# Kernel tuning notes

Measured on AMD Instinct MI355X. Metric: run time of the kernel, lower is better.

The kernel has to match this reference:

```python
import jax, jax.numpy as jnp
import numpy as np

N = 50000        # nodes
E = 800000       # edges (avg degree 16)
G = 512          # graphs in batch
H = 128          # hidden_channels
F = 128          # num_filters
NG = 50          # num_gaussians
NI = 6           # num_interactions
CUTOFF = 10.0


def ssp(x):
    # shifted softplus: softplus(x) - log(2)
    return jax.nn.softplus(x) - jnp.log(2.0).astype(x.dtype)


def setup_inputs() -> dict:
    key = jax.random.key(0)
    ks = jax.random.split(key, 16)
    z = jax.random.randint(ks[0], (N,), 0, 100)
    pos = jax.random.uniform(ks[1], (N, 3), jnp.float32) * 5.0  # box keeps d < cutoff
    batch = jnp.sort(jax.random.randint(ks[2], (N,), 0, G))
    row = jax.random.randint(ks[3], (E,), 0, N)
    off = jax.random.randint(ks[4], (E,), 1, N)
    col = (row + off) % N  # no self loops -> d > 0
    edge_index = jnp.stack([row, col])
    s = 0.1
    emb = jax.random.normal(ks[5], (100, H), jnp.float32) * s
    w1 = jax.random.normal(ks[6], (NI, NG, F), jnp.float32) * s
    b1 = jnp.zeros((NI, F), jnp.float32)
    w2 = jax.random.normal(ks[7], (NI, F, F), jnp.float32) * s
    b2 = jnp.zeros((NI, F), jnp.float32)
    lin1_w = jax.random.normal(ks[8], (NI, H, F), jnp.float32) * s   # no bias
    lin2_w = jax.random.normal(ks[9], (NI, F, H), jnp.float32) * s
    lin2_b = jnp.zeros((NI, H), jnp.float32)
    lin_w = jax.random.normal(ks[10], (NI, H, H), jnp.float32) * s
    lin_b = jnp.zeros((NI, H), jnp.float32)
    out_w1 = jax.random.normal(ks[11], (H, H // 2), jnp.float32) * s
    out_b1 = jnp.zeros((H // 2,), jnp.float32)
    out_w2 = jax.random.normal(ks[12], (H // 2, 1), jnp.float32) * s
    out_b2 = jnp.zeros((1,), jnp.float32)
    return dict(pos=pos, emb=emb, w1=w1, b1=b1, w2=w2, b2=b2,
                lin1_w=lin1_w, lin2_w=lin2_w, lin2_b=lin2_b,
                lin_w=lin_w, lin_b=lin_b,
                out_w1=out_w1, out_b1=out_b1, out_w2=out_w2, out_b2=out_b2,
                z=z, batch=batch, edge_index=edge_index)


def reference(pos, emb, w1, b1, w2, b2, lin1_w, lin2_w, lin2_b, lin_w, lin_b,
              out_w1, out_b1, out_w2, out_b2, z, batch, edge_index):
    row, col = edge_index[0], edge_index[1]  # row = target i, col = source j
    diff = pos[row] - pos[col]               # [E,3]
    d = jnp.sqrt(jnp.sum(diff * diff, axis=-1) + 1e-12)  # [E]

    # Gaussian smearing (PyG): exp(coeff * (d - offset)^2)
    offset = jnp.linspace(0.0, CUTOFF, NG, dtype=jnp.float32)
    coeff = -0.5 / (offset[1] - offset[0]) ** 2
    rbf = jnp.exp(coeff * (d[:, None] - offset) ** 2)  # [E,NG]

    # cosine cutoff
    C = 0.5 * (jnp.cos(d * (jnp.pi / CUTOFF)) + 1.0)    # [E]

    h = emb[z]  # [N,H]
    for i in range(NI):
        # filter network on edge RBF features
        W = ssp(rbf @ w1[i] + b1[i]) @ w2[i] + b2[i]    # [E,F]
        W = W * C[:, None]
        x = h @ lin1_w[i]                               # [N,F]
        msg = x[col] * W                                # gather + modulate [E,F]
        agg = jax.ops.segment_sum(msg, row, num_segments=N)  # scatter-add [N,F]
        x = agg @ lin2_w[i] + lin2_b[i]                 # [N,H]
        x = ssp(x)
        x = x @ lin_w[i] + lin_b[i]
        h = h + x                                       # residual

    h = ssp(h @ out_w1 + out_b1)                        # [N,H//2]
    per_atom = h @ out_w2 + out_b2                      # [N,1]
    energy = jax.ops.segment_sum(per_atom, batch, num_segments=G)  # [G,1]
    return energy
```

## Files before the change

kernel.cpp:

```cpp
#include <hip/hip_runtime.h>
#include <math.h>


constexpr int Nn  = 50000;
constexpr int Ee  = 800000;
constexpr int Gg  = 512;
constexpr int Hh  = 128;
constexpr int NGg = 50;
constexpr int NIi = 6;
constexpr int TS  = 4096;
constexpr float DMAXv = 8.6603f;

typedef short bf16x8 __attribute__((ext_vector_type(8)));
typedef float f32x4  __attribute__((ext_vector_type(4)));

__device__ __forceinline__ float ssp(float v) {
    return log1pf(__expf(-fabsf(v))) + fmaxf(v, 0.0f) - 0.69314718056f;
}
__device__ __forceinline__ unsigned short f2bf(float f) {
    unsigned int u = __float_as_uint(f);
    u += 0x7fffu + ((u >> 16) & 1u);
    return (unsigned short)(u >> 16);
}
__device__ __forceinline__ float bf2f(unsigned int h) {
    return __uint_as_float(h << 16);
}

__global__ void k_embed(const float* __restrict__ emb, const int* __restrict__ z,
                        float* __restrict__ h) {
    int tid = blockIdx.x * 256 + threadIdx.x;
    int n = tid >> 7, f = tid & 127;
    h[tid] = emb[z[n] * Hh + f];
}

__global__ void k_hist(const int* __restrict__ ei, int* __restrict__ counts) {
    int e = blockIdx.x * 256 + threadIdx.x;
    if (e >= Ee) return;
    atomicAdd(&counts[ei[e]], 1);
}

__global__ __launch_bounds__(1024) void k_scan(const int* __restrict__ counts,
                                               int* __restrict__ offsets) {
    __shared__ int s[1024];
    constexpr int CH = (Nn + 1023) / 1024;
    int t = threadIdx.x;
    int beg = t * CH, end = beg + CH; if (end > Nn) end = Nn;
    int sum = 0;
    for (int i = beg; i < end; ++i) sum += counts[i];
    s[t] = sum;
    __syncthreads();
    for (int off = 1; off < 1024; off <<= 1) {
        int v = (t >= off) ? s[t - off] : 0;
        __syncthreads();
        s[t] += v;
        __syncthreads();
    }
    int base = (t == 0) ? 0 : s[t - 1];
    for (int i = beg; i < end; ++i) {
        offsets[i] = base;
        base += counts[i];
    }
    if (t == 1023) offsets[Nn] = base;
}

__global__ void k_scatter(const int* __restrict__ ei, const float* __restrict__ pos,
                          int* __restrict__ cursor, int2* __restrict__ payload,
                          float inv_step) {
    int e = blockIdx.x * 256 + threadIdx.x;
    if (e >= Ee) return;
    int r = ei[e], c = ei[Ee + e];
    float dx = pos[3 * r    ] - pos[3 * c    ];
    float dy = pos[3 * r + 1] - pos[3 * c + 1];
    float dz = pos[3 * r + 2] - pos[3 * c + 2];
    float d = sqrtf(dx * dx + dy * dy + dz * dz + 1e-12f);
    float u = d * inv_step;
    if (u > (float)(TS - 1) - 5e-4f) u = (float)(TS - 1) - 5e-4f;
    int p = atomicAdd(&cursor[r], 1);
    payload[p] = make_int2(c, __float_as_int(u));
}

__global__ void k_pack(const float* __restrict__ lin1, const float* __restrict__ lin2,
                       const float* __restrict__ lin3, const float* __restrict__ ow1,
                       short* __restrict__ Wp) {
    int o = blockIdx.x * 256 + threadIdx.x;
    if (o < 18 * 16384) {
        int m = o >> 14, r = o & 16383;
        int k = (r >> 7) & 127, c = r & 127;
        int i = m / 3, which = m % 3;
        const float* src = which == 0 ? lin1 : (which == 1 ? lin2 : lin3);
        float v = src[(size_t)i * 16384 + k * 128 + c];
        int nt = c >> 4, lc = c & 15, kk = k >> 5, kg = (k >> 3) & 3, e = k & 7;
        int l = kg * 16 + lc;
        Wp[(size_t)m * 16384 + ((nt * 4 + kk) * 64 + l) * 8 + e] = (short)f2bf(v);
    } else {
        int r = o - 18 * 16384;
        int k = r >> 6, c = r & 63;
        float v = ow1[k * 64 + c];
        int nt = c >> 4, lc = c & 15, kk = k >> 5, kg = (k >> 3) & 3, e = k & 7;
        int l = kg * 16 + lc;
        Wp[(size_t)18 * 16384 + ((nt * 4 + kk) * 64 + l) * 8 + e] = (short)f2bf(v);
    }
}

__global__ __launch_bounds__(256) void k_table(
        const float* __restrict__ w1, const float* __restrict__ b1,
        const float* __restrict__ w2, const float* __restrict__ b2,
        unsigned short* __restrict__ T, float step) {
    __shared__ unsigned int w2p[64 * 128];
    __shared__ unsigned int w1p[25 * 128];
    __shared__ float rbf_s[2][NGg];
    __shared__ float tb[2][128];
    int tid = threadIdx.x;
    for (int i = tid; i < 64 * 128; i += 256) {
        int k2 = i >> 7, f = i & 127;
        unsigned int lo = f2bf(w2[(2 * k2) * 128 + f]);
        unsigned int hi = f2bf(w2[(2 * k2 + 1) * 128 + f]);
        w2p[i] = lo | (hi << 16);
    }
    for (int i = tid; i < 25 * 128; i += 256) {
        int k2 = i >> 7, f = i & 127;
        unsigned int lo = f2bf(w1[(2 * k2) * 128 + f]);
        unsigned int hi = f2bf(w1[(2 * k2 + 1) * 128 + f]);
        w1p[i] = lo | (hi << 16);
    }
    int jj = tid >> 7, f = tid & 127;
    float bb1 = b1[f], bb2 = b2[f];
    for (int p = 0; p < 4; ++p) {
        int j = blockIdx.x * 8 + p * 2 + jj;
        float dj = j * step;
        __syncthreads();
        if (f < NGg) {
            float u = dj - f * (10.0f / 49.0f);
            rbf_s[jj][f] = expf(-12.00500f * u * u);
        }
        __syncthreads();
        float u = bb1;
        for (int k2 = 0; k2 < 25; ++k2) {
            unsigned int wv = w1p[k2 * 128 + f];
            u = fmaf(rbf_s[jj][2 * k2    ], bf2f(wv & 0xffffu), u);
            u = fmaf(rbf_s[jj][2 * k2 + 1], bf2f(wv >> 16), u);
        }
        tb[jj][f] = ssp(u);
        __syncthreads();
        float w = bb2;
        for (int k2 = 0; k2 < 64; ++k2) {
            unsigned int wv = w2p[k2 * 128 + f];
            w = fmaf(tb[jj][2 * k2    ], bf2f(wv & 0xffffu), w);
            w = fmaf(tb[jj][2 * k2 + 1], bf2f(wv >> 16), w);
        }
        float C = 0.5f * (cosf(dj * 0.31415926535f) + 1.0f);
        T[j * 128 + f] = f2bf(w * C);
    }
}

__global__ __launch_bounds__(256) void k_mfma1(
        const float* __restrict__ in, const short* __restrict__ Wp,
        unsigned short* __restrict__ out, int nrows) {
    __shared__ short As[64 * 128];
    int tid = threadIdx.x;
    int base = blockIdx.x * 64;
    const float4* in4 = (const float4*)(in + (size_t)base * 128);
    int lim4 = (nrows - base) * 32;
    for (int i = tid; i < 2048; i += 256) {
        float4 v = make_float4(0.f, 0.f, 0.f, 0.f);
        if (i < lim4) v = in4[i];
        ushort4 o; o.x = f2bf(v.x); o.y = f2bf(v.y); o.z = f2bf(v.z); o.w = f2bf(v.w);
        int row = i >> 5, colg = i & 31;
        int byte = (row * 256 + colg * 8) ^ ((row & 7) << 4);
        *(ushort4*)((char*)As + byte) = o;
    }
    __syncthreads();

    int w = tid >> 6, lane = tid & 63;
    int arow = w * 16 + (lane & 15);
    bf16x8 a[4];
    #pragma unroll
    for (int kk = 0; kk < 4; ++kk) {
        int byte = (arow * 256 + kk * 64 + (lane >> 4) * 16) ^ ((arow & 7) << 4);
        a[kk] = *(const bf16x8*)((const char*)As + byte);
    }
    f32x4 acc[8];
    f32x4 zero = {0.f, 0.f, 0.f, 0.f};
    #pragma unroll
    for (int nt = 0; nt < 8; ++nt) acc[nt] = zero;
    const bf16x8* Wp8 = (const bf16x8*)Wp;
    #pragma unroll
    for (int nt = 0; nt < 8; ++nt)
        #pragma unroll
        for (int kk = 0; kk < 4; ++kk)
            acc[nt] = __builtin_amdgcn_mfma_f32_16x16x32_bf16(
                a[kk], Wp8[(nt * 4 + kk) * 64 + lane], acc[nt], 0, 0, 0);
    #pragma unroll
    for (int nt = 0; nt < 8; ++nt) {
        int col = nt * 16 + (lane & 15);
        #pragma unroll
        for (int r = 0; r < 4; ++r) {
            int row = base + w * 16 + (lane >> 4) * 4 + r;
            if (row < nrows) out[(size_t)row * 128 + col] = f2bf(acc[nt][r]);
        }
    }
}

__global__ __launch_bounds__(256) void k_mfma23(
        const float* __restrict__ agg, const short* __restrict__ W2p,
        const float* __restrict__ b2, const short* __restrict__ W3p,
        const float* __restrict__ b3, float* __restrict__ h, int nrows) {
    __shared__ short As[64 * 128];
    int tid = threadIdx.x;
    int base = blockIdx.x * 64;
    const float4* in4 = (const float4*)(agg + (size_t)base * 128);
    int lim4 = (nrows - base) * 32;
    for (int i = tid; i < 2048; i += 256) {
        float4 v = make_float4(0.f, 0.f, 0.f, 0.f);
        if (i < lim4) v = in4[i];
        ushort4 o; o.x = f2bf(v.x); o.y = f2bf(v.y); o.z = f2bf(v.z); o.w = f2bf(v.w);
        int row = i >> 5, colg = i & 31;
        int byte = (row * 256 + colg * 8) ^ ((row & 7) << 4);
        *(ushort4*)((char*)As + byte) = o;
    }
    __syncthreads();

    int w = tid >> 6, lane = tid & 63;
    int arow = w * 16 + (lane & 15);
    f32x4 zero = {0.f, 0.f, 0.f, 0.f};
    bf16x8 a[4];
    #pragma unroll
    for (int kk = 0; kk < 4; ++kk) {
        int byte = (arow * 256 + kk * 64 + (lane >> 4) * 16) ^ ((arow & 7) << 4);
        a[kk] = *(const bf16x8*)((const char*)As + byte);
    }
    f32x4 acc[8];
    #pragma unroll
    for (int nt = 0; nt < 8; ++nt) acc[nt] = zero;
    const bf16x8* W2p8 = (const bf16x8*)W2p;
    #pragma unroll
    for (int nt = 0; nt < 8; ++nt)
        #pragma unroll
        for (int kk = 0; kk < 4; ++kk)
            acc[nt] = __builtin_amdgcn_mfma_f32_16x16x32_bf16(
                a[kk], W2p8[(nt * 4 + kk) * 64 + lane], acc[nt], 0, 0, 0);

    #pragma unroll
    for (int nt = 0; nt < 8; ++nt) {
        int col = nt * 16 + (lane & 15);
        float bv = b2[col];
        #pragma unroll
        for (int r = 0; r < 4; ++r) {
            int row = w * 16 + (lane >> 4) * 4 + r;
            int byte = (row * 256 + col * 2) ^ ((row & 7) << 4);
            *(unsigned short*)((char*)As + byte) = f2bf(ssp(acc[nt][r] + bv));
        }
    }
    __syncthreads();

    bf16x8 a2[4];
    #pragma unroll
    for (int kk = 0; kk < 4; ++kk) {
        int byte = (arow * 256 + kk * 64 + (lane >> 4) * 16) ^ ((arow & 7) << 4);
        a2[kk] = *(const bf16x8*)((const char*)As + byte);
    }
    f32x4 acc2[8];
    #pragma unroll
    for (int nt = 0; nt < 8; ++nt) acc2[nt] = zero;
    const bf16x8* W3p8 = (const bf16x8*)W3p;
    #pragma unroll
    for (int nt = 0; nt < 8; ++nt)
        #pragma unroll
        for (int kk = 0; kk < 4; ++kk)
            acc2[nt] = __builtin_amdgcn_mfma_f32_16x16x32_bf16(
                a2[kk], W3p8[(nt * 4 + kk) * 64 + lane], acc2[nt], 0, 0, 0);

    #pragma unroll
    for (int nt = 0; nt < 8; ++nt) {
        int col = nt * 16 + (lane & 15);
        float bv3 = b3[col];
        #pragma unroll
        for (int r = 0; r < 4; ++r) {
            int row = base + w * 16 + (lane >> 4) * 4 + r;
            if (row < nrows) {
                float* hp = h + (size_t)row * 128 + col;
                *hp += acc2[nt][r] + bv3;
            }
        }
    }
}

__device__ __forceinline__ void lerp_acc(unsigned int ta, unsigned int tb,
                                         unsigned int xv, float fr, float2& acc) {
    float t0a = bf2f(ta & 0xffffu), t0b = bf2f(ta >> 16);
    float t1a = bf2f(tb & 0xffffu), t1b = bf2f(tb >> 16);
    acc.x = fmaf(bf2f(xv & 0xffffu), fmaf(t1a - t0a, fr, t0a), acc.x);
    acc.y = fmaf(bf2f(xv >> 16),     fmaf(t1b - t0b, fr, t0b), acc.y);
}

__global__ __launch_bounds__(256) void k_agg(
        const int* __restrict__ offs, const int2* __restrict__ payload,
        const unsigned int* __restrict__ xw, const unsigned int* __restrict__ Tw,
        float* __restrict__ agg) {
    int wid = threadIdx.x >> 6, lane = threadIdx.x & 63;
    int n = blockIdx.x * 4 + wid;
    int beg = offs[n], end = offs[n + 1];
    float2 acc = make_float2(0.f, 0.f);
    int e = beg, cnt = end - beg;
    int2 p0, p1, p2, p3;
    if (cnt >= 4) { p0 = payload[e]; p1 = payload[e + 1]; p2 = payload[e + 2]; p3 = payload[e + 3]; }
    while (cnt >= 4) {
        unsigned int c0 = p0.x, c1 = p1.x, c2 = p2.x, c3 = p3.x;
        float u0 = __int_as_float(p0.y), u1 = __int_as_float(p1.y);
        float u2 = __int_as_float(p2.y), u3 = __int_as_float(p3.y);
        int j0 = (int)u0, j1 = (int)u1, j2 = (int)u2, j3 = (int)u3;
        float f0 = u0 - j0, f1 = u1 - j1, f2 = u2 - j2, f3 = u3 - j3;
        unsigned int ta0 = Tw[j0 * 64 + lane], tb0 = Tw[j0 * 64 + 64 + lane];
        unsigned int ta1 = Tw[j1 * 64 + lane], tb1 = Tw[j1 * 64 + 64 + lane];
        unsigned int ta2 = Tw[j2 * 64 + lane], tb2 = Tw[j2 * 64 + 64 + lane];
        unsigned int ta3 = Tw[j3 * 64 + lane], tb3 = Tw[j3 * 64 + 64 + lane];
        unsigned int xv0 = xw[(size_t)c0 * 64 + lane];
        unsigned int xv1 = xw[(size_t)c1 * 64 + lane];
        unsigned int xv2 = xw[(size_t)c2 * 64 + lane];
        unsigned int xv3 = xw[(size_t)c3 * 64 + lane];
        e += 4; cnt -= 4;
        if (cnt >= 4) { p0 = payload[e]; p1 = payload[e + 1]; p2 = payload[e + 2]; p3 = payload[e + 3]; }
        lerp_acc(ta0, tb0, xv0, f0, acc);
        lerp_acc(ta1, tb1, xv1, f1, acc);
        lerp_acc(ta2, tb2, xv2, f2, acc);
        lerp_acc(ta3, tb3, xv3, f3, acc);
    }
    for (; cnt > 0; --cnt, ++e) {
        int2 cur = payload[e];
        float u = __int_as_float(cur.y);
        int j = (int)u;
        float fr = u - (float)j;
        unsigned int ta = Tw[j * 64 + lane];
        unsigned int tb = Tw[j * 64 + 64 + lane];
        unsigned int xv = xw[(size_t)cur.x * 64 + lane];
        lerp_acc(ta, tb, xv, fr, acc);
    }
    ((float2*)agg)[(size_t)n * 64 + lane] = acc;
}

__global__ __launch_bounds__(256) void k_out(
        const float* __restrict__ h, const short* __restrict__ OW1p,
        const float* __restrict__ ob1, const float* __restrict__ ow2,
        const float* __restrict__ ob2, const int* __restrict__ batch,
        float* __restrict__ energy, int nrows) {
    __shared__ short As[64 * 128];
    __shared__ float rowsum[64];
    int tid = threadIdx.x;
    int base = blockIdx.x * 64;
    const float4* in4 = (const float4*)(h + (size_t)base * 128);
    int lim4 = (nrows - base) * 32;
    for (int i = tid; i < 2048; i += 256) {
        float4 v = make_float4(0.f, 0.f, 0.f, 0.f);
        if (i < lim4) v = in4[i];
        ushort4 o; o.x = f2bf(v.x); o.y = f2bf(v.y); o.z = f2bf(v.z); o.w = f2bf(v.w);
        int row = i >> 5, colg = i & 31;
        int byte = (row * 256 + colg * 8) ^ ((row & 7) << 4);
        *(ushort4*)((char*)As + byte) = o;
    }
    __syncthreads();

    int w = tid >> 6, lane = tid & 63;
    int arow = w * 16 + (lane & 15);
    bf16x8 a[4];
    #pragma unroll
    for (int kk = 0; kk < 4; ++kk) {
        int byte = (arow * 256 + kk * 64 + (lane >> 4) * 16) ^ ((arow & 7) << 4);
        a[kk] = *(const bf16x8*)((const char*)As + byte);
    }
    f32x4 acc[4];
    f32x4 zero = {0.f, 0.f, 0.f, 0.f};
    #pragma unroll
    for (int nt = 0; nt < 4; ++nt) acc[nt] = zero;
    const bf16x8* W8 = (const bf16x8*)OW1p;
    #pragma unroll
    for (int nt = 0; nt < 4; ++nt)
        #pragma unroll
        for (int kk = 0; kk < 4; ++kk)
            acc[nt] = __builtin_amdgcn_mfma_f32_16x16x32_bf16(
                a[kk], W8[(nt * 4 + kk) * 64 + lane], acc[nt], 0, 0, 0);

    float p[4] = {0.f, 0.f, 0.f, 0.f};
    #pragma unroll
    for (int nt = 0; nt < 4; ++nt) {
        int col = nt * 16 + (lane & 15);
        float b = ob1[col], wv = ow2[col];
        #pragma unroll
        for (int r = 0; r < 4; ++r) p[r] += ssp(acc[nt][r] + b) * wv;
    }
    #pragma unroll
    for (int m = 1; m < 16; m <<= 1) {
        #pragma unroll
        for (int r = 0; r < 4; ++r) p[r] += __shfl_xor(p[r], m);
    }
    if ((lane & 15) == 0) {
        #pragma unroll
        for (int r = 0; r < 4; ++r) rowsum[w * 16 + (lane >> 4) * 4 + r] = p[r];
    }
    __syncthreads();
    if (tid < 64) {
        int row = base + tid;
        int rc = row < nrows ? row : nrows - 1;
        int g = batch[rc];
        float v = (row < nrows) ? rowsum[tid] + ob2[0] : 0.f;
        #pragma unroll
        for (int off = 1; off < 64; off <<= 1) {
            float vo = __shfl_down(v, off);
            int   go = __shfl_down(g, off);
            if (tid + off < 64 && go == g) v += vo;
        }
        int gp = __shfl_up(g, 1);
        if (row < nrows && (tid == 0 || gp != g))
            unsafeAtomicAdd(&energy[g], v);
    }
}

extern "C" void kernel_launch(void* const* d_in, const int* in_sizes, int n_in,
                              void* d_out, int out_size, void* d_ws, size_t ws_size,
                              hipStream_t stream) {
    const float* pos    = (const float*)d_in[0];
    const float* emb    = (const float*)d_in[1];
    const float* w1     = (const float*)d_in[2];
    const float* b1     = (const float*)d_in[3];
    const float* w2     = (const float*)d_in[4];
    const float* b2     = (const float*)d_in[5];
    const float* lin1_w = (const float*)d_in[6];
    const float* lin2_w = (const float*)d_in[7];
    const float* lin2_b = (const float*)d_in[8];
    const float* lin_w  = (const float*)d_in[9];
    const float* lin_b  = (const float*)d_in[10];
    const float* ow1    = (const float*)d_in[11];
    const float* ob1    = (const float*)d_in[12];
    const float* ow2    = (const float*)d_in[13];
    const float* ob2    = (const float*)d_in[14];
    const int*   z      = (const int*)d_in[15];
    const int*   batch  = (const int*)d_in[16];
    const int*   ei     = (const int*)d_in[17];
    float* energy = (float*)d_out;

    char* ws = (char*)d_ws;
    float*          h       = (float*)ws;          ws += (size_t)Nn * 128 * 4;
    float*          agg     = (float*)ws;          ws += (size_t)Nn * 128 * 4;
    unsigned short* xb      = (unsigned short*)ws; ws += (size_t)Nn * 128 * 2;
    unsigned short* T       = (unsigned short*)ws; ws += (size_t)TS * 128 * 2;
    int2*           payload = (int2*)ws;           ws += (size_t)Ee * 8;
    short*          Wp      = (short*)ws;          ws += ((size_t)18 * 16384 + 8192) * 2;
    int*            counts  = (int*)ws;            ws += (size_t)Nn * 4;
    int*            offsets = (int*)ws;            ws += (size_t)(Nn + 1) * 4;
    int*            cursor  = (int*)ws;            ws += (size_t)Nn * 4;

    float step = DMAXv / (TS - 1);
    float inv_step = (TS - 1) / DMAXv;

    hipMemsetAsync(d_out, 0, Gg * 4, stream);
    hipMemsetAsync(counts, 0, (size_t)Nn * 4, stream);
    k_embed<<<Nn * 128 / 256, 256, 0, stream>>>(emb, z, h);

    k_hist<<<(Ee + 255) / 256, 256, 0, stream>>>(ei, counts);
    k_scan<<<1, 1024, 0, stream>>>(counts, offsets);
    hipMemcpyAsync(cursor, offsets, (size_t)Nn * 4, hipMemcpyDeviceToDevice, stream);
    k_scatter<<<(Ee + 255) / 256, 256, 0, stream>>>(ei, pos, cursor, payload, inv_step);

    k_pack<<<(18 * 16384 + 8192) / 256, 256, 0, stream>>>(lin1_w, lin2_w, lin_w, ow1, Wp);

    int gemm_blocks = (Nn + 63) / 64;
    for (int i = 0; i < NIi; ++i) {
        const short* W1p = Wp + (size_t)(i * 3 + 0) * 16384;
        const short* W2p = Wp + (size_t)(i * 3 + 1) * 16384;
        const short* W3p = Wp + (size_t)(i * 3 + 2) * 16384;
        k_table<<<512, 256, 0, stream>>>(w1 + (size_t)i * NGg * 128, b1 + (size_t)i * 128,
                                         w2 + (size_t)i * 128 * 128, b2 + (size_t)i * 128,
                                         T, step);
        k_mfma1<<<gemm_blocks, 256, 0, stream>>>(h, W1p, xb, Nn);
        k_agg<<<Nn / 4, 256, 0, stream>>>(offsets, payload,
                                          (const unsigned int*)xb, (const unsigned int*)T, agg);
        k_mfma23<<<gemm_blocks, 256, 0, stream>>>(agg, W2p, lin2_b + (size_t)i * Hh,
                                                  W3p, lin_b + (size_t)i * Hh, h, Nn);
    }
    k_out<<<gemm_blocks, 256, 0, stream>>>(h, Wp + (size_t)18 * 16384,
                                           ob1, ow2, ob2, batch, energy, Nn);
}
```

Measured before the change: 1.018 ms.

## Fuse next-layer lin1 GEMM and output head into post-aggregation kernel; parallelize scan

Fuses the next interaction's lin1 projection (and, on the last layer, the output MLP and per-graph energy reduction) into the post-aggregation GEMM kernel. The updated h stays in shared memory as bf16 instead of being re-read by a separate kernel. This removes the k_mfma1 and k_out launches and their full passes over h. The single-block serial prefix scan plus device memcpy is replaced by a three-kernel multi-block scan that writes offsets and cursor together, and the filter-table build is reordered so it runs after aggregation. One cost is that the next layer's lin1 input is now rounded from an fp32 value computed inside the kernel, not re-read from h.

```diff
diff --git a/kernel.cpp b/kernel.cpp
--- a/kernel.cpp
+++ b/kernel.cpp
@@ -9,6 +9,7 @@
 constexpr int NGg = 50;
 constexpr int NIi = 6;
 constexpr int TS  = 4096;
+constexpr int NB  = (Nn + 255) / 256;
 constexpr float DMAXv = 8.6603f;
 
 typedef short bf16x8 __attribute__((ext_vector_type(8)));
@@ -39,28 +40,58 @@
     atomicAdd(&counts[ei[e]], 1);
 }
 
-__global__ __launch_bounds__(1024) void k_scan(const int* __restrict__ counts,
-                                               int* __restrict__ offsets) {
-    __shared__ int s[1024];
-    constexpr int CH = (Nn + 1023) / 1024;
+__global__ __launch_bounds__(256) void k_scanA(const int* __restrict__ counts,
+                                               int* __restrict__ incl,
+                                               int* __restrict__ bsum) {
+    int t = blockIdx.x * 256 + threadIdx.x;
+    int lane = threadIdx.x & 63, wv = threadIdx.x >> 6;
+    int c = (t < Nn) ? counts[t] : 0;
+    int v = c;
+    #pragma unroll
+    for (int off = 1; off < 64; off <<= 1) {
+        int u = __shfl_up(v, off);
+        if (lane >= off) v += u;
+    }
+    __shared__ int ws[4];
+    if (lane == 63) ws[wv] = v;
+    __syncthreads();
+    if (threadIdx.x == 0) {
+        int s = 0;
+        #pragma unroll
+        for (int i = 0; i < 4; ++i) { int x = ws[i]; ws[i] = s; s += x; }
+        bsum[blockIdx.x] = s;
+    }
+    __syncthreads();
+    v += ws[wv];
+    if (t < Nn) incl[t] = v;
+}
+
+__global__ __launch_bounds__(256) void k_scanB(int* __restrict__ bsum) {
+    __shared__ int s[256];
     int t = threadIdx.x;
-    int beg = t * CH, end = beg + CH; if (end > Nn) end = Nn;
-    int sum = 0;
-    for (int i = beg; i < end; ++i) sum += counts[i];
-    s[t] = sum;
-    __syncthreads();
-    for (int off = 1; off < 1024; off <<= 1) {
-        int v = (t >= off) ? s[t - off] : 0;
+    int v = (t < NB) ? bsum[t] : 0;
+    s[t] = v;
+    __syncthreads();
+    for (int off = 1; off < 256; off <<= 1) {
+        int u = (t >= off) ? s[t - off] : 0;
         __syncthreads();
-        s[t] += v;
+        s[t] += u;
         __syncthreads();
     }
-    int base = (t == 0) ? 0 : s[t - 1];
-    for (int i = beg; i < end; ++i) {
-        offsets[i] = base;
-        base += counts[i];
-    }
-    if (t == 1023) offsets[Nn] = base;
+    if (t < NB) bsum[t] = s[t] - v;
+}
+
+__global__ __launch_bounds__(256) void k_scanC(const int* __restrict__ counts,
+                                               const int* __restrict__ incl,
+                                               const int* __restrict__ bsum,
+                                               int* __restrict__ offsets,
+                                               int* __restrict__ cursor) {
+    int t = blockIdx.x * 256 + threadIdx.x;
+    if (t >= Nn) return;
+    int off = bsum[blockIdx.x] + incl[t] - counts[t];
+    offsets[t] = off;
+    cursor[t]  = off;
+    if (t == Nn - 1) offsets[Nn] = off + counts[t];
 }
 
 __global__ void k_scatter(const int* __restrict__ ei, const float* __restrict__ pos,
@@ -201,11 +232,16 @@
     }
 }
 
-__global__ __launch_bounds__(256) void k_mfma23(
+__global__ __launch_bounds__(256) void k_fused(
         const float* __restrict__ agg, const short* __restrict__ W2p,
         const float* __restrict__ b2, const short* __restrict__ W3p,
-        const float* __restrict__ b3, float* __restrict__ h, int nrows) {
+        const float* __restrict__ b3, float* __restrict__ h,
+        const short* __restrict__ Wnext, unsigned short* __restrict__ xb,
+        const short* __restrict__ OW1p, const float* __restrict__ ob1,
+        const float* __restrict__ ow2, const float* __restrict__ ob2,
+        const int* __restrict__ batch, float* __restrict__ energy, int nrows) {
     __shared__ short As[64 * 128];
+    __shared__ float rowsum[64];
     int tid = threadIdx.x;
     int base = blockIdx.x * 64;
     const float4* in4 = (const float4*)(agg + (size_t)base * 128);
@@ -270,17 +306,95 @@
             acc2[nt] = __builtin_amdgcn_mfma_f32_16x16x32_bf16(
                 a2[kk], W3p8[(nt * 4 + kk) * 64 + lane], acc2[nt], 0, 0, 0);
 
+    bool last = (OW1p != nullptr);
     #pragma unroll
     for (int nt = 0; nt < 8; ++nt) {
         int col = nt * 16 + (lane & 15);
         float bv3 = b3[col];
         #pragma unroll
         for (int r = 0; r < 4; ++r) {
-            int row = base + w * 16 + (lane >> 4) * 4 + r;
-            if (row < nrows) {
-                float* hp = h + (size_t)row * 128 + col;
-                *hp += acc2[nt][r] + bv3;
+            int lrow = w * 16 + (lane >> 4) * 4 + r;
+            int row = base + lrow;
+            float hv = 0.f;
+            if (row < nrows) hv = h[(size_t)row * 128 + col];
+            float nv = hv + acc2[nt][r] + bv3;
+            if (!last && row < nrows) h[(size_t)row * 128 + col] = nv;
+            int byte = (lrow * 256 + col * 2) ^ ((lrow & 7) << 4);
+            *(unsigned short*)((char*)As + byte) = f2bf(nv);
+        }
+    }
+    __syncthreads();
+
+    bf16x8 a3[4];
+    #pragma unroll
+    for (int kk = 0; kk < 4; ++kk) {
+        int byte = (arow * 256 + kk * 64 + (lane >> 4) * 16) ^ ((arow & 7) << 4);
+        a3[kk] = *(const bf16x8*)((const char*)As + byte);
+    }
+
+    if (!last) {
+        f32x4 acc3[8];
+        #pragma unroll
+        for (int nt = 0; nt < 8; ++nt) acc3[nt] = zero;
+        const bf16x8* Wn8 = (const bf16x8*)Wnext;
+        #pragma unroll
+        for (int nt = 0; nt < 8; ++nt)
+            #pragma unroll
+            for (int kk = 0; kk < 4; ++kk)
+                acc3[nt] = __builtin_amdgcn_mfma_f32_16x16x32_bf16(
+                    a3[kk], Wn8[(nt * 4 + kk) * 64 + lane], acc3[nt], 0, 0, 0);
+        #pragma unroll
+        for (int nt = 0; nt < 8; ++nt) {
+            int col = nt * 16 + (lane & 15);
+            #pragma unroll
+            for (int r = 0; r < 4; ++r) {
+                int row = base + w * 16 + (lane >> 4) * 4 + r;
+                if (row < nrows) xb[(size_t)row * 128 + col] = f2bf(acc3[nt][r]);
             }
+        }
+    } else {
+        f32x4 acc4[4];
+        #pragma unroll
+        for (int nt = 0; nt < 4; ++nt) acc4[nt] = zero;
+        const bf16x8* W8 = (const bf16x8*)OW1p;
+        #pragma unroll
+        for (int nt = 0; nt < 4; ++nt)
+            #pragma unroll
+            for (int kk = 0; kk < 4; ++kk)
+                acc4[nt] = __builtin_amdgcn_mfma_f32_16x16x32_bf16(
+                    a3[kk], W8[(nt * 4 + kk) * 64 + lane], acc4[nt], 0, 0, 0);
+        float p[4] = {0.f, 0.f, 0.f, 0.f};
+        #pragma unroll
+        for (int nt = 0; nt < 4; ++nt) {
+            int col = nt * 16 + (lane & 15);
+            float b = ob1[col], wv = ow2[col];
+            #pragma unroll
+            for (int r = 0; r < 4; ++r) p[r] += ssp(acc4[nt][r] + b) * wv;
+        }
+        #pragma unroll
+        for (int m = 1; m < 16; m <<= 1) {
+            #pragma unroll
+            for (int r = 0; r < 4; ++r) p[r] += __shfl_xor(p[r], m);
+        }
+        if ((lane & 15) == 0) {
+            #pragma unroll
+            for (int r = 0; r < 4; ++r) rowsum[w * 16 + (lane >> 4) * 4 + r] = p[r];
+        }
+        __syncthreads();
+        if (tid < 64) {
+            int row = base + tid;
+            int rc = row < nrows ? row : nrows - 1;
+            int g = batch[rc];
+            float v = (row < nrows) ? rowsum[tid] + ob2[0] : 0.f;
+            #pragma unroll
+            for (int off = 1; off < 64; off <<= 1) {
+                float vo = __shfl_down(v, off);
+                int   go = __shfl_down(g, off);
+                if (tid + off < 64 && go == g) v += vo;
+            }
+            int gp = __shfl_up(g, 1);
+            if (row < nrows && (tid == 0 || gp != g))
+                unsafeAtomicAdd(&energy[g], v);
         }
     }
 }
@@ -338,82 +452,6 @@
     ((float2*)agg)[(size_t)n * 64 + lane] = acc;
 }
 
-__global__ __launch_bounds__(256) void k_out(
-        const float* __restrict__ h, const short* __restrict__ OW1p,
-        const float* __restrict__ ob1, const float* __restrict__ ow2,
-        const float* __restrict__ ob2, const int* __restrict__ batch,
-        float* __restrict__ energy, int nrows) {
-    __shared__ short As[64 * 128];
-    __shared__ float rowsum[64];
-    int tid = threadIdx.x;
-    int base = blockIdx.x * 64;
-    const float4* in4 = (const float4*)(h + (size_t)base * 128);
-    int lim4 = (nrows - base) * 32;
-    for (int i = tid; i < 2048; i += 256) {
-        float4 v = make_float4(0.f, 0.f, 0.f, 0.f);
-        if (i < lim4) v = in4[i];
-        ushort4 o; o.x = f2bf(v.x); o.y = f2bf(v.y); o.z = f2bf(v.z); o.w = f2bf(v.w);
-        int row = i >> 5, colg = i & 31;
-        int byte = (row * 256 + colg * 8) ^ ((row & 7) << 4);
-        *(ushort4*)((char*)As + byte) = o;
-    }
-    __syncthreads();
-
-    int w = tid >> 6, lane = tid & 63;
-    int arow = w * 16 + (lane & 15);
-    bf16x8 a[4];
-    #pragma unroll
-    for (int kk = 0; kk < 4; ++kk) {
-        int byte = (arow * 256 + kk * 64 + (lane >> 4) * 16) ^ ((arow & 7) << 4);
-        a[kk] = *(const bf16x8*)((const char*)As + byte);
-    }
-    f32x4 acc[4];
-    f32x4 zero = {0.f, 0.f, 0.f, 0.f};
-    #pragma unroll
-    for (int nt = 0; nt < 4; ++nt) acc[nt] = zero;
-    const bf16x8* W8 = (const bf16x8*)OW1p;
-    #pragma unroll
-    for (int nt = 0; nt < 4; ++nt)
-        #pragma unroll
-        for (int kk = 0; kk < 4; ++kk)
-            acc[nt] = __builtin_amdgcn_mfma_f32_16x16x32_bf16(
-                a[kk], W8[(nt * 4 + kk) * 64 + lane], acc[nt], 0, 0, 0);
-
-    float p[4] = {0.f, 0.f, 0.f, 0.f};
-    #pragma unroll
-    for (int nt = 0; nt < 4; ++nt) {
-        int col = nt * 16 + (lane & 15);
-        float b = ob1[col], wv = ow2[col];
-        #pragma unroll
-        for (int r = 0; r < 4; ++r) p[r] += ssp(acc[nt][r] + b) * wv;
-    }
-    #pragma unroll
-    for (int m = 1; m < 16; m <<= 1) {
-        #pragma unroll
-        for (int r = 0; r < 4; ++r) p[r] += __shfl_xor(p[r], m);
-    }
-    if ((lane & 15) == 0) {
-        #pragma unroll
-        for (int r = 0; r < 4; ++r) rowsum[w * 16 + (lane >> 4) * 4 + r] = p[r];
-    }
-    __syncthreads();
-    if (tid < 64) {
-        int row = base + tid;
-        int rc = row < nrows ? row : nrows - 1;
-        int g = batch[rc];
-        float v = (row < nrows) ? rowsum[tid] + ob2[0] : 0.f;
-        #pragma unroll
-        for (int off = 1; off < 64; off <<= 1) {
-            float vo = __shfl_down(v, off);
-            int   go = __shfl_down(g, off);
-            if (tid + off < 64 && go == g) v += vo;
-        }
-        int gp = __shfl_up(g, 1);
-        if (row < nrows && (tid == 0 || gp != g))
-            unsafeAtomicAdd(&energy[g], v);
-    }
-}
-
 extern "C" void kernel_launch(void* const* d_in, const int* in_sizes, int n_in,
                               void* d_out, int out_size, void* d_ws, size_t ws_size,
                               hipStream_t stream) {
@@ -447,6 +485,8 @@
     int*            counts  = (int*)ws;            ws += (size_t)Nn * 4;
     int*            offsets = (int*)ws;            ws += (size_t)(Nn + 1) * 4;
     int*            cursor  = (int*)ws;            ws += (size_t)Nn * 4;
+    int*            incl    = (int*)ws;            ws += (size_t)Nn * 4;
+    int*            bsum    = (int*)ws;            ws += (size_t)256 * 4;
 
     float step = DMAXv / (TS - 1);
     float inv_step = (TS - 1) / DMAXv;
@@ -456,26 +496,34 @@
     k_embed<<<Nn * 128 / 256, 256, 0, stream>>>(emb, z, h);
 
     k_hist<<<(Ee + 255) / 256, 256, 0, stream>>>(ei, counts);
-    k_scan<<<1, 1024, 0, stream>>>(counts, offsets);
-    hipMemcpyAsync(cursor, offsets, (size_t)Nn * 4, hipMemcpyDeviceToDevice, stream);
+    k_scanA<<<NB, 256, 0, stream>>>(counts, incl, bsum);
+    k_scanB<<<1, 256, 0, stream>>>(bsum);
+    k_scanC<<<NB, 256, 0, stream>>>(counts, incl, bsum, offsets, cursor);
     k_scatter<<<(Ee + 255) / 256, 256, 0, stream>>>(ei, pos, cursor, payload, inv_step);
 
     k_pack<<<(18 * 16384 + 8192) / 256, 256, 0, stream>>>(lin1_w, lin2_w, lin_w, ow1, Wp);
 
     int gemm_blocks = (Nn + 63) / 64;
+    const short* OWp = Wp + (size_t)18 * 16384;
+
+    k_table<<<512, 256, 0, stream>>>(w1, b1, w2, b2, T, step);
+    k_mfma1<<<gemm_blocks, 256, 0, stream>>>(h, Wp, xb, Nn);
+
     for (int i = 0; i < NIi; ++i) {
-        const short* W1p = Wp + (size_t)(i * 3 + 0) * 16384;
         const short* W2p = Wp + (size_t)(i * 3 + 1) * 16384;
         const short* W3p = Wp + (size_t)(i * 3 + 2) * 16384;
-        k_table<<<512, 256, 0, stream>>>(w1 + (size_t)i * NGg * 128, b1 + (size_t)i * 128,
-                                         w2 + (size_t)i * 128 * 128, b2 + (size_t)i * 128,
-                                         T, step);
-        k_mfma1<<<gemm_blocks, 256, 0, stream>>>(h, W1p, xb, Nn);
+        bool last = (i == NIi - 1);
+        const short* Wnext = last ? nullptr : Wp + (size_t)((i + 1) * 3) * 16384;
+
         k_agg<<<Nn / 4, 256, 0, stream>>>(offsets, payload,
                                           (const unsigned int*)xb, (const unsigned int*)T, agg);
-        k_mfma23<<<gemm_blocks, 256, 0, stream>>>(agg, W2p, lin2_b + (size_t)i * Hh,
-                                                  W3p, lin_b + (size_t)i * Hh, h, Nn);
-    }
-    k_out<<<gemm_blocks, 256, 0, stream>>>(h, Wp + (size_t)18 * 16384,
-                                           ob1, ow2, ob2, batch, energy, Nn);
-}
+        if (!last)
+            k_table<<<512, 256, 0, stream>>>(w1 + (size_t)(i + 1) * NGg * 128,
+                                             b1 + (size_t)(i + 1) * 128,
+                                             w2 + (size_t)(i + 1) * 128 * 128,
+                                             b2 + (size_t)(i + 1) * 128, T, step);
+        k_fused<<<gemm_blocks, 256, 0, stream>>>(
+            agg, W2p, lin2_b + (size_t)i * Hh, W3p, lin_b + (size_t)i * Hh, h,
+            Wnext, xb, last ? OWp : nullptr, ob1, ow2, ob2, batch, energy, Nn);
+    }
+}
```

Measured after the change: 949.7 us. -6.7%, faster.
